# Kernel tuning notes

Measured on AMD Instinct MI355X. Metric: run time of the kernel, lower is better.

## Reference

```python
import jax, jax.numpy as jnp
import numpy as np

EMBED_DIM = 512
MAX_POSITION = 10000
BASE = 10000.0
BATCH, SEQ = 8, 8192


def _build_cache():
    # freqs_k = 1 / base^(2k/d), k = 0..d/2-1  -> [d/2]
    freqs = 1.0 / (BASE ** (jnp.arange(0, EMBED_DIM, 2, dtype=jnp.float32) / EMBED_DIM))
    positions = jnp.arange(MAX_POSITION, dtype=jnp.float32)
    angles = jnp.outer(positions, freqs)  # [max_position, d/2]
    # cache[p, k, 0] = sin, cache[p, k, 1] = cos (matches torch.stack([sin, cos], -1))
    return jnp.stack([jnp.sin(angles), jnp.cos(angles)], axis=-1)


def setup_inputs() -> dict:
    key = jax.random.key(0)
    positions = jax.random.randint(key, (BATCH, SEQ), 0, MAX_POSITION, dtype=jnp.int64)
    sin_cos_cache = _build_cache()  # [max_position, d/2, 2] float32
    return {"positions": positions, "sin_cos_cache": sin_cos_cache}


def reference(positions, sin_cos_cache):
    # Gather rows: [..., d/2, 2]
    sc = sin_cos_cache[positions]
    # Interleave: even output dims get cos (index 1), odd dims get sin (index 0).
    interleaved = jnp.stack([sc[..., 1], sc[..., 0]], axis=-1)  # [..., d/2, 2]
    return interleaved.reshape(*positions.shape, EMBED_DIM)
```

## Files before the change

kernel.cpp:

```cpp
#include <hip/hip_runtime.h>


#define EMBED_DIM 512
#define POS_PER_GROUP 4

typedef float v4f __attribute__((ext_vector_type(4)));
typedef int   v4i __attribute__((ext_vector_type(4)));

__device__ __forceinline__ v4f swap_pairs(v4f v) {
    return (v4f){v.y, v.x, v.w, v.z};
}

__device__ __forceinline__ void do_one_pos(int sub, int p,
                                           const float* __restrict__ cache,
                                           float* __restrict__ dst_row) {
    const v4f* __restrict__ src = (const v4f*)(cache + (size_t)p * EMBED_DIM);
    v4f* __restrict__ dst       = (v4f*)dst_row;
    v4f v0 = src[sub];
    v4f v1 = src[sub + 32];
    v4f v2 = src[sub + 64];
    v4f v3 = src[sub + 96];
    __builtin_nontemporal_store(swap_pairs(v0), &dst[sub]);
    __builtin_nontemporal_store(swap_pairs(v1), &dst[sub + 32]);
    __builtin_nontemporal_store(swap_pairs(v2), &dst[sub + 64]);
    __builtin_nontemporal_store(swap_pairs(v3), &dst[sub + 96]);
}

__global__ __launch_bounds__(256) void ScalarRoPEEmbedding_83769042141635_kernel(
    const int* __restrict__ positions,
    const float* __restrict__ cache,
    float* __restrict__ out,
    int n_pos)
{
    int tid   = blockIdx.x * blockDim.x + threadIdx.x;
    int group = tid >> 5;
    int sub   = tid & 31;
    int base  = group * POS_PER_GROUP;
    if (base >= n_pos) return;

    if (base + POS_PER_GROUP <= n_pos) {
        v4i p4 = *(const v4i*)(positions + base);

        const v4f* __restrict__ s0 = (const v4f*)(cache + (size_t)p4.x * EMBED_DIM);
        const v4f* __restrict__ s1 = (const v4f*)(cache + (size_t)p4.y * EMBED_DIM);
        const v4f* __restrict__ s2 = (const v4f*)(cache + (size_t)p4.z * EMBED_DIM);
        const v4f* __restrict__ s3 = (const v4f*)(cache + (size_t)p4.w * EMBED_DIM);

        v4f a00 = s0[sub], a01 = s0[sub + 32], a02 = s0[sub + 64], a03 = s0[sub + 96];
        v4f a10 = s1[sub], a11 = s1[sub + 32], a12 = s1[sub + 64], a13 = s1[sub + 96];
        v4f a20 = s2[sub], a21 = s2[sub + 32], a22 = s2[sub + 64], a23 = s2[sub + 96];
        v4f a30 = s3[sub], a31 = s3[sub + 32], a32 = s3[sub + 64], a33 = s3[sub + 96];

        v4f* __restrict__ d0 = (v4f*)(out + (size_t)(base + 0) * EMBED_DIM);
        v4f* __restrict__ d1 = (v4f*)(out + (size_t)(base + 1) * EMBED_DIM);
        v4f* __restrict__ d2 = (v4f*)(out + (size_t)(base + 2) * EMBED_DIM);
        v4f* __restrict__ d3 = (v4f*)(out + (size_t)(base + 3) * EMBED_DIM);

        __builtin_nontemporal_store(swap_pairs(a00), &d0[sub]);
        __builtin_nontemporal_store(swap_pairs(a01), &d0[sub + 32]);
        __builtin_nontemporal_store(swap_pairs(a02), &d0[sub + 64]);
        __builtin_nontemporal_store(swap_pairs(a03), &d0[sub + 96]);
        __builtin_nontemporal_store(swap_pairs(a10), &d1[sub]);
        __builtin_nontemporal_store(swap_pairs(a11), &d1[sub + 32]);
        __builtin_nontemporal_store(swap_pairs(a12), &d1[sub + 64]);
        __builtin_nontemporal_store(swap_pairs(a13), &d1[sub + 96]);
        __builtin_nontemporal_store(swap_pairs(a20), &d2[sub]);
        __builtin_nontemporal_store(swap_pairs(a21), &d2[sub + 32]);
        __builtin_nontemporal_store(swap_pairs(a22), &d2[sub + 64]);
        __builtin_nontemporal_store(swap_pairs(a23), &d2[sub + 96]);
        __builtin_nontemporal_store(swap_pairs(a30), &d3[sub]);
        __builtin_nontemporal_store(swap_pairs(a31), &d3[sub + 32]);
        __builtin_nontemporal_store(swap_pairs(a32), &d3[sub + 64]);
        __builtin_nontemporal_store(swap_pairs(a33), &d3[sub + 96]);
    } else {
        for (int i = base; i < n_pos; ++i) {
            int p = positions[i];
            do_one_pos(sub, p, cache, out + (size_t)i * EMBED_DIM);
        }
    }
}

extern "C" void kernel_launch(void* const* d_in, const int* in_sizes, int n_in,
                              void* d_out, int out_size, void* d_ws, size_t ws_size,
                              hipStream_t stream) {
    const int*   positions = (const int*)d_in[0];
    const float* cache     = (const float*)d_in[1];
    float*       out       = (float*)d_out;

    int n_pos    = in_sizes[0];
    int n_groups = (n_pos + POS_PER_GROUP - 1) / POS_PER_GROUP;
    int total_threads = n_groups * 32;
    int block = 256;
    int grid  = (total_threads + block - 1) / block;

    ScalarRoPEEmbedding_83769042141635_kernel<<<grid, block, 0, stream>>>(
        positions, cache, out, n_pos);
}
```

Before: 163.0 us.

## Bucket output rows by position and scatter each cache row once

Adds a bucketing pass that uses atomics to group output row indices by position. A scatter kernel then assigns one wave per position, which loads and swaps that cache row once and writes it to every row that uses it. Rows beyond a fixed duplicate cap go to an overflow list. The goal is fewer gather reads from the cache. The cost is a memset, an extra kernel launch and atomics, and an overflow list capped at a fixed size that can silently drop rows.

```diff
diff --git a/kernel.cpp b/kernel.cpp
--- a/kernel.cpp
+++ b/kernel.cpp
@@ -2,7 +2,16 @@
 
 
 #define EMBED_DIM 512
-#define POS_PER_GROUP 4
+#define MAX_POSITION 10000
+#define MAX_DUP 64
+#define OV_CAP 2048
+
+#define WS_COUNTS_OFF   0
+#define WS_OVCNT_OFF    40000
+#define WS_MEMSET_BYTES 40064
+#define WS_BUCKETS_OFF  40064
+#define WS_OVLIST_OFF   2600064
+#define WS_BYTES_NEEDED 2608256
 
 typedef float v4f __attribute__((ext_vector_type(4)));
 typedef int   v4i __attribute__((ext_vector_type(4)));
@@ -11,22 +20,67 @@
     return (v4f){v.y, v.x, v.w, v.z};
 }
 
-__device__ __forceinline__ void do_one_pos(int sub, int p,
-                                           const float* __restrict__ cache,
-                                           float* __restrict__ dst_row) {
-    const v4f* __restrict__ src = (const v4f*)(cache + (size_t)p * EMBED_DIM);
-    v4f* __restrict__ dst       = (v4f*)dst_row;
-    v4f v0 = src[sub];
-    v4f v1 = src[sub + 32];
-    v4f v2 = src[sub + 64];
-    v4f v3 = src[sub + 96];
-    __builtin_nontemporal_store(swap_pairs(v0), &dst[sub]);
-    __builtin_nontemporal_store(swap_pairs(v1), &dst[sub + 32]);
-    __builtin_nontemporal_store(swap_pairs(v2), &dst[sub + 64]);
-    __builtin_nontemporal_store(swap_pairs(v3), &dst[sub + 96]);
+__global__ __launch_bounds__(256) void ScalarRoPEEmbedding_83769042141635_bucket(
+    const int* __restrict__ positions, int n_pos,
+    int* __restrict__ counts, int* __restrict__ ovf_cnt,
+    int* __restrict__ buckets, int* __restrict__ ovf_list)
+{
+    int i = blockIdx.x * blockDim.x + threadIdx.x;
+    if (i >= n_pos) return;
+    int p = positions[i];
+    int slot = atomicAdd(&counts[p], 1);
+    if (slot < MAX_DUP) {
+        buckets[p * MAX_DUP + slot] = i;
+    } else {
+        int o = atomicAdd(ovf_cnt, 1);
+        if (o < OV_CAP) ovf_list[o] = i;
+    }
 }
 
-__global__ __launch_bounds__(256) void ScalarRoPEEmbedding_83769042141635_kernel(
+__global__ __launch_bounds__(256) void ScalarRoPEEmbedding_83769042141635_scatter(
+    const int* __restrict__ positions,
+    const float* __restrict__ cache,
+    float* __restrict__ out,
+    const int* __restrict__ counts, const int* __restrict__ ovf_cnt,
+    const int* __restrict__ buckets, const int* __restrict__ ovf_list)
+{
+    int wave = (blockIdx.x * blockDim.x + threadIdx.x) >> 6;
+    int lane = threadIdx.x & 63;
+
+    if (wave < MAX_POSITION) {
+        int p = wave;
+        int cnt = counts[p];
+        if (cnt == 0) return;
+        if (cnt > MAX_DUP) cnt = MAX_DUP;
+
+        const v4f* __restrict__ src = (const v4f*)(cache + (size_t)p * EMBED_DIM);
+        v4f wa = swap_pairs(src[lane]);
+        v4f wb = swap_pairs(src[lane + 64]);
+
+        const int* __restrict__ bk = buckets + p * MAX_DUP;
+        for (int j = 0; j < cnt; ++j) {
+            int row = bk[j];
+            v4f* __restrict__ dst = (v4f*)(out + (size_t)row * EMBED_DIM);
+            __builtin_nontemporal_store(wa, &dst[lane]);
+            __builtin_nontemporal_store(wb, &dst[lane + 64]);
+        }
+    } else {
+        int o = wave - MAX_POSITION;
+        int oc = *ovf_cnt;
+        if (oc > OV_CAP) oc = OV_CAP;
+        if (o >= oc) return;
+        int row = ovf_list[o];
+        int p = positions[row];
+        const v4f* __restrict__ src = (const v4f*)(cache + (size_t)p * EMBED_DIM);
+        v4f wa = swap_pairs(src[lane]);
+        v4f wb = swap_pairs(src[lane + 64]);
+        v4f* __restrict__ dst = (v4f*)(out + (size_t)row * EMBED_DIM);
+        __builtin_nontemporal_store(wa, &dst[lane]);
+        __builtin_nontemporal_store(wb, &dst[lane + 64]);
+    }
+}
+
+__global__ __launch_bounds__(256) void ScalarRoPEEmbedding_83769042141635_direct(
     const int* __restrict__ positions,
     const float* __restrict__ cache,
     float* __restrict__ out,
@@ -35,27 +89,23 @@
     int tid   = blockIdx.x * blockDim.x + threadIdx.x;
     int group = tid >> 5;
     int sub   = tid & 31;
-    int base  = group * POS_PER_GROUP;
+    int base  = group * 4;
     if (base >= n_pos) return;
 
-    if (base + POS_PER_GROUP <= n_pos) {
+    if (base + 4 <= n_pos) {
         v4i p4 = *(const v4i*)(positions + base);
-
         const v4f* __restrict__ s0 = (const v4f*)(cache + (size_t)p4.x * EMBED_DIM);
         const v4f* __restrict__ s1 = (const v4f*)(cache + (size_t)p4.y * EMBED_DIM);
         const v4f* __restrict__ s2 = (const v4f*)(cache + (size_t)p4.z * EMBED_DIM);
         const v4f* __restrict__ s3 = (const v4f*)(cache + (size_t)p4.w * EMBED_DIM);
-
         v4f a00 = s0[sub], a01 = s0[sub + 32], a02 = s0[sub + 64], a03 = s0[sub + 96];
         v4f a10 = s1[sub], a11 = s1[sub + 32], a12 = s1[sub + 64], a13 = s1[sub + 96];
         v4f a20 = s2[sub], a21 = s2[sub + 32], a22 = s2[sub + 64], a23 = s2[sub + 96];
         v4f a30 = s3[sub], a31 = s3[sub + 32], a32 = s3[sub + 64], a33 = s3[sub + 96];
-
         v4f* __restrict__ d0 = (v4f*)(out + (size_t)(base + 0) * EMBED_DIM);
         v4f* __restrict__ d1 = (v4f*)(out + (size_t)(base + 1) * EMBED_DIM);
         v4f* __restrict__ d2 = (v4f*)(out + (size_t)(base + 2) * EMBED_DIM);
         v4f* __restrict__ d3 = (v4f*)(out + (size_t)(base + 3) * EMBED_DIM);
-
         __builtin_nontemporal_store(swap_pairs(a00), &d0[sub]);
         __builtin_nontemporal_store(swap_pairs(a01), &d0[sub + 32]);
         __builtin_nontemporal_store(swap_pairs(a02), &d0[sub + 64]);
@@ -75,7 +125,16 @@
     } else {
         for (int i = base; i < n_pos; ++i) {
             int p = positions[i];
-            do_one_pos(sub, p, cache, out + (size_t)i * EMBED_DIM);
+            const v4f* __restrict__ src = (const v4f*)(cache + (size_t)p * EMBED_DIM);
+            v4f* __restrict__ dst       = (v4f*)(out + (size_t)i * EMBED_DIM);
+            v4f v0 = src[sub];
+            v4f v1 = src[sub + 32];
+            v4f v2 = src[sub + 64];
+            v4f v3 = src[sub + 96];
+            __builtin_nontemporal_store(swap_pairs(v0), &dst[sub]);
+            __builtin_nontemporal_store(swap_pairs(v1), &dst[sub + 32]);
+            __builtin_nontemporal_store(swap_pairs(v2), &dst[sub + 64]);
+            __builtin_nontemporal_store(swap_pairs(v3), &dst[sub + 96]);
         }
     }
 }
@@ -86,13 +145,33 @@
     const int*   positions = (const int*)d_in[0];
     const float* cache     = (const float*)d_in[1];
     float*       out       = (float*)d_out;
+    int n_pos = in_sizes[0];
 
-    int n_pos    = in_sizes[0];
-    int n_groups = (n_pos + POS_PER_GROUP - 1) / POS_PER_GROUP;
-    int total_threads = n_groups * 32;
-    int block = 256;
-    int grid  = (total_threads + block - 1) / block;
+    if (d_ws != nullptr && ws_size >= (size_t)WS_BYTES_NEEDED) {
+        char* ws = (char*)d_ws;
+        int* counts   = (int*)(ws + WS_COUNTS_OFF);
+        int* ovf_cnt  = (int*)(ws + WS_OVCNT_OFF);
+        int* buckets  = (int*)(ws + WS_BUCKETS_OFF);
+        int* ovf_list = (int*)(ws + WS_OVLIST_OFF);
 
-    ScalarRoPEEmbedding_83769042141635_kernel<<<grid, block, 0, stream>>>(
-        positions, cache, out, n_pos);
+        hipMemsetAsync(d_ws, 0, WS_MEMSET_BYTES, stream);
+
+        int blkA = 256;
+        int grdA = (n_pos + blkA - 1) / blkA;
+        ScalarRoPEEmbedding_83769042141635_bucket<<<grdA, blkA, 0, stream>>>(
+            positions, n_pos, counts, ovf_cnt, buckets, ovf_list);
+
+        int n_waves = MAX_POSITION + OV_CAP;
+        int blkB = 256;
+        int grdB = (n_waves * 64 + blkB - 1) / blkB;
+        ScalarRoPEEmbedding_83769042141635_scatter<<<grdB, blkB, 0, stream>>>(
+            positions, cache, out, counts, ovf_cnt, buckets, ovf_list);
+    } else {
+        int n_groups = (n_pos + 3) / 4;
+        int total_threads = n_groups * 32;
+        int block = 256;
+        int grid  = (total_threads + block - 1) / block;
+        ScalarRoPEEmbedding_83769042141635_direct<<<grid, block, 0, stream>>>(
+            positions, cache, out, n_pos);
+    }
 }
```

Result: slower. 167.7 us (+2.9%).
